# Optimization experiments

Hardware: AMD Instinct MI355X
Metric: run time of the kernel (lower is better)

The kernel has to match this reference:

```python
import jax, jax.numpy as jnp
import numpy as np

P, Q, R, H1, H2, PH, B = 32, 32, 8, 128, 64, 16, 8192
PAIRS = P * Q
OUT = PAIRS * R  # X_Z_layer output units


def _pairwise_mask(p, q, r):
    # rows i*q+k correspond to pair (x_i, z_k): connected to x_i and z_k only
    mx = np.zeros((p * q, p), np.float32)
    for i in range(p):
        mx[i * q:(i + 1) * q, i] = 1.0
    mz = np.tile(np.eye(q, dtype=np.float32), (p, 1))
    m = np.concatenate([mx, mz], axis=1)          # [p*q, p+q]
    return np.repeat(m, r, axis=0)                 # [p*q*r, p+q]


def setup_inputs() -> dict:
    key = jax.random.key(0)
    ks = jax.random.split(key, 24)
    rn = lambda k, s, sc=0.1: jax.random.normal(k, s, jnp.float32) * sc
    x = jax.random.normal(ks[0], (B, P), jnp.float32)
    z = jax.random.normal(ks[1], (B, Q), jnp.float32)
    # X_mlp: P -> H1 -> H2 -> 1
    xw1, xb1 = rn(ks[2], (P, H1)), rn(ks[3], (H1,))
    xw2, xb2 = rn(ks[4], (H1, H2)), rn(ks[5], (H2,))
    xw3, xb3 = rn(ks[6], (H2, 1)), rn(ks[7], (1,))
    # Z_mlp: Q -> H1 -> H2 -> 1
    zw1, zb1 = rn(ks[8], (Q, H1)), rn(ks[9], (H1,))
    zw2, zb2 = rn(ks[10], (Q if False else H1, H2)), rn(ks[11], (H2,))
    zw3, zb3 = rn(ks[12], (H2, 1)), rn(ks[13], (1,))
    # masked X_Z_layer: weight pre-multiplied by structured mask (as in __init__)
    mask = jnp.asarray(_pairwise_mask(P, Q, R))    # [OUT, P+Q]
    xzw = (rn(ks[14], (OUT, P + Q)) * mask).T      # [P+Q, OUT]
    xzb = rn(ks[15], (OUT,))
    # 1024 tiny per-pair MLPs: R -> PH (bias) -> 1 (no bias), stacked
    pw1 = rn(ks[16], (PAIRS, R, PH))
    pb1 = rn(ks[17], (PAIRS, PH))
    pw2 = rn(ks[18], (PAIRS, PH))
    return dict(x=x, z=z, xw1=xw1, xb1=xb1, xw2=xw2, xb2=xb2, xw3=xw3, xb3=xb3,
                zw1=zw1, zb1=zb1, zw2=zw2, zb2=zb2, zw3=zw3, zb3=zb3,
                xzw=xzw, xzb=xzb, pw1=pw1, pb1=pb1, pw2=pw2)


def reference(x, z, xw1, xb1, xw2, xb2, xw3, xb3,
              zw1, zb1, zw2, zb2, zw3, zb3, xzw, xzb, pw1, pb1, pw2):
    relu = jax.nn.relu
    # main-effect MLPs
    hx = relu(relu(x @ xw1 + xb1) @ xw2 + xb2)
    out_x = hx @ xw3 + xb3                         # [B,1]
    hz = relu(relu(z @ zw1 + zb1) @ zw2 + zb2)
    out_z = hz @ zw3 + zb3                         # [B,1]
    # masked interaction layer
    xz = jnp.concatenate([x, z], axis=1)           # [B, P+Q]
    h = relu(xz @ xzw + xzb)                       # [B, OUT]
    # all 1024 per-pair MLPs as one batched GEMM
    hp = h.reshape(h.shape[0], PAIRS, R)           # [B, pairs, R]
    t = relu(jnp.einsum('bpr,prh->bph', hp, pw1) + pb1)
    out_xz = jnp.einsum('bph,ph->b', t, pw2)[:, None]  # sum over pairs -> [B,1]
    return out_x + out_z + out_xz
```

## Files before the change

### kernel.cpp

```cpp
#include <hip/hip_runtime.h>

#define B_TOT 8192
#define PP 32
#define QQ 32
#define RR 8
#define H1 128
#define H2 64
#define PHH 16
#define PAIRS 1024
#define OUT_UNITS 8192

#define NBLK_MM 256
#define NBLK_IA 2048

typedef float f32x16 __attribute__((ext_vector_type(16)));
typedef short s16x8  __attribute__((ext_vector_type(8)));

union FragU { s16x8 v; unsigned int u[4]; };

__device__ inline unsigned int pack_bf16(float lo, float hi) {
    return __builtin_amdgcn_perm(__float_as_uint(hi), __float_as_uint(lo), 0x07060302u);
}

union SharedU {
    union {
        struct {
            float zT[16][256];
            float4 lwx[16][2];
            float4 lwz[16][2];
            float4 lhb[16][2];
            unsigned lpw1T[17][16][4];
            float lpb[16][16];
            float lpw2[16][16];
        } s;
        float red[256][33];
    } ia;
    struct {
        float h1T[128][65];
        float red2[8][64];
    } mm;
};

__global__ __launch_bounds__(512, 4) void fused_k(
    const float* __restrict__ x, const float* __restrict__ z,
    const float* __restrict__ xw1, const float* __restrict__ xb1,
    const float* __restrict__ xw2, const float* __restrict__ xb2,
    const float* __restrict__ xw3, const float* __restrict__ xb3,
    const float* __restrict__ zw1, const float* __restrict__ zb1,
    const float* __restrict__ zw2, const float* __restrict__ zb2,
    const float* __restrict__ zw3, const float* __restrict__ zb3,
    const float* __restrict__ xzw, const float* __restrict__ xzb,
    const float* __restrict__ pw1, const float* __restrict__ pb1,
    const float* __restrict__ pw2, float* __restrict__ out)
{
    __shared__ SharedU sh;
    const int bid  = blockIdx.x;
    const int t    = threadIdx.x;
    const int w    = t >> 6;
    const int lane = t & 63;

    if (bid >= NBLK_MM) {
        const int ib    = bid - NBLK_MM;
        const int bx    = ib & 31;
        const int y     = ib >> 5;
        const int m     = lane & 31;
        const int kh    = lane >> 5;
        const int jj    = m & 15;
        const int cph   = m >> 4;
        const int b0    = bx * 256;
        const int i_x   = y >> 1;
        const int k0    = (y & 1) * 16;
        const int pair0 = y * 16;

        {
            int row = t >> 1;
            int c8  = (t & 1) * 8;
            const float* src = z + (size_t)(b0 + row) * 32 + k0 + c8;
            float4 a4 = *reinterpret_cast<const float4*>(src);
            float4 b4 = *reinterpret_cast<const float4*>(src + 4);
            sh.ia.s.zT[c8+0][row] = a4.x; sh.ia.s.zT[c8+1][row] = a4.y;
            sh.ia.s.zT[c8+2][row] = a4.z; sh.ia.s.zT[c8+3][row] = a4.w;
            sh.ia.s.zT[c8+4][row] = b4.x; sh.ia.s.zT[c8+5][row] = b4.y;
            sh.ia.s.zT[c8+6][row] = b4.z; sh.ia.s.zT[c8+7][row] = b4.w;
        }
        if (t < 128) {
            int p = t >> 3, c = t & 7;
            int gp = pair0 + p;
            reinterpret_cast<float*>(sh.ia.s.lwx)[t] = xzw[(size_t)i_x * OUT_UNITS + gp*8 + c];
            reinterpret_cast<float*>(sh.ia.s.lwz)[t] = xzw[(size_t)(32 + k0 + p) * OUT_UNITS + gp*8 + c];
            reinterpret_cast<float*>(sh.ia.s.lhb)[t] = xzb[gp*8 + c];
        }
        if (t < 256) {
            int p = t >> 4, j = t & 15;
            int gp = pair0 + p;
            sh.ia.s.lpb[p][j]  = pb1[gp*PHH + j];
            sh.ia.s.lpw2[p][j] = pw2[gp*PHH + j];
        }
        #pragma unroll
        for (int it = 0; it < 2; ++it) {
            int idx = t + it * 512;
            int p = idx >> 6, u = (idx >> 4) & 3, j = idx & 15;
            int gp = pair0 + p;
            float lo = pw1[(size_t)gp * 128 + (2*u)*16 + j];
            float hi = pw1[(size_t)gp * 128 + (2*u+1)*16 + j];
            sh.ia.s.lpw1T[p][j][u] = pack_bf16(lo, hi);
        }
        if (t < 64) reinterpret_cast<unsigned*>(sh.ia.s.lpw1T[16])[t] = 0u;

        const int g   = w >> 1;
        const int pph = w & 1;
        const int bl  = g * 64 + m;
        const float xv0 = x[(size_t)(b0 + bl)      * 32 + i_x];
        const float xv1 = x[(size_t)(b0 + bl + 32) * 32 + i_x];
        __syncthreads();

        f32x16 acc0, acc1;
        #pragma unroll
        for (int r = 0; r < 16; ++r) { acc0[r] = 0.f; acc1[r] = 0.f; }

        const bool realB = (kh == cph);

        #pragma unroll 2
        for (int kk = 0; kk < 4; ++kk) {
            const int ppl = pph * 4 + kk;
            const int pAl = 2*ppl + kh;
            const int pBl = 2*ppl + cph;

            const float zv0 = sh.ia.s.zT[pAl][bl];
            const float zv1 = sh.ia.s.zT[pAl][bl + 32];
            const float4 wxa = sh.ia.s.lwx[pAl][0], wxb = sh.ia.s.lwx[pAl][1];
            const float4 wza = sh.ia.s.lwz[pAl][0], wzb = sh.ia.s.lwz[pAl][1];
            const float4 hba = sh.ia.s.lhb[pAl][0], hbb = sh.ia.s.lhb[pAl][1];

            float h0[8], h1v[8];
            h0[0] = fmaxf(fmaf(xv0, wxa.x, fmaf(zv0, wza.x, hba.x)), 0.f);
            h0[1] = fmaxf(fmaf(xv0, wxa.y, fmaf(zv0, wza.y, hba.y)), 0.f);
            h0[2] = fmaxf(fmaf(xv0, wxa.z, fmaf(zv0, wza.z, hba.z)), 0.f);
            h0[3] = fmaxf(fmaf(xv0, wxa.w, fmaf(zv0, wza.w, hba.w)), 0.f);
            h0[4] = fmaxf(fmaf(xv0, wxb.x, fmaf(zv0, wzb.x, hbb.x)), 0.f);
            h0[5] = fmaxf(fmaf(xv0, wxb.y, fmaf(zv0, wzb.y, hbb.y)), 0.f);
            h0[6] = fmaxf(fmaf(xv0, wxb.z, fmaf(zv0, wzb.z, hbb.z)), 0.f);
            h0[7] = fmaxf(fmaf(xv0, wxb.w, fmaf(zv0, wzb.w, hbb.w)), 0.f);
            h1v[0] = fmaxf(fmaf(xv1, wxa.x, fmaf(zv1, wza.x, hba.x)), 0.f);
            h1v[1] = fmaxf(fmaf(xv1, wxa.y, fmaf(zv1, wza.y, hba.y)), 0.f);
            h1v[2] = fmaxf(fmaf(xv1, wxa.z, fmaf(zv1, wza.z, hba.z)), 0.f);
            h1v[3] = fmaxf(fmaf(xv1, wxa.w, fmaf(zv1, wza.w, hba.w)), 0.f);
            h1v[4] = fmaxf(fmaf(xv1, wxb.x, fmaf(zv1, wzb.x, hbb.x)), 0.f);
            h1v[5] = fmaxf(fmaf(xv1, wxb.y, fmaf(zv1, wzb.y, hbb.y)), 0.f);
            h1v[6] = fmaxf(fmaf(xv1, wxb.z, fmaf(zv1, wzb.z, hbb.z)), 0.f);
            h1v[7] = fmaxf(fmaf(xv1, wxb.w, fmaf(zv1, wzb.w, hbb.w)), 0.f);

            FragU a0, a1, bf;
            a0.u[0] = pack_bf16(h0[0], h0[1]);
            a0.u[1] = pack_bf16(h0[2], h0[3]);
            a0.u[2] = pack_bf16(h0[4], h0[5]);
            a0.u[3] = pack_bf16(h0[6], h0[7]);
            a1.u[0] = pack_bf16(h1v[0], h1v[1]);
            a1.u[1] = pack_bf16(h1v[2], h1v[3]);
            a1.u[2] = pack_bf16(h1v[4], h1v[5]);
            a1.u[3] = pack_bf16(h1v[6], h1v[7]);

            const unsigned* bq = sh.ia.s.lpw1T[realB ? pBl : 16][jj];
            bf.u[0] = bq[0]; bf.u[1] = bq[1]; bf.u[2] = bq[2]; bf.u[3] = bq[3];

            const float pbv = sh.ia.s.lpb[pBl][jj];
            const float w2v = sh.ia.s.lpw2[pBl][jj];

            f32x16 cpb;
            #pragma unroll
            for (int r = 0; r < 16; ++r) cpb[r] = pbv;

            f32x16 d0 = __builtin_amdgcn_mfma_f32_32x32x16_bf16(a0.v, bf.v, cpb, 0, 0, 0);
            f32x16 d1 = __builtin_amdgcn_mfma_f32_32x32x16_bf16(a1.v, bf.v, cpb, 0, 0, 0);

            #pragma unroll
            for (int r = 0; r < 16; ++r)
                acc0[r] = fmaf(fmaxf(d0[r], 0.f), w2v, acc0[r]);
            #pragma unroll
            for (int r = 0; r < 16; ++r)
                acc1[r] = fmaf(fmaxf(d1[r], 0.f), w2v, acc1[r]);
        }

        __syncthreads();
        const int rbase = g * 64;
        if (pph == 0) {
            #pragma unroll
            for (int r = 0; r < 16; ++r) {
                int rowf = (r & 3) + 8 * (r >> 2) + 4 * kh;
                sh.ia.red[rbase + rowf][m]      = acc0[r];
                sh.ia.red[rbase + 32 + rowf][m] = acc1[r];
            }
        }
        __syncthreads();
        if (pph == 1) {
            #pragma unroll
            for (int r = 0; r < 16; ++r) {
                int rowf = (r & 3) + 8 * (r >> 2) + 4 * kh;
                sh.ia.red[rbase + rowf][m]      += acc0[r];
                sh.ia.red[rbase + 32 + rowf][m] += acc1[r];
            }
        }
        __syncthreads();
        if (t < 256) {
            float s = 0.f;
            #pragma unroll
            for (int c = 0; c < 32; ++c) s += sh.ia.red[t][c];
            atomicAdd(out + b0 + t, s);
        }
    } else {
        const int btile = bid & 127;
        const int which = bid >> 7;
        const float* in = which ? z   : x;
        const float* w1 = which ? zw1 : xw1;
        const float* b1 = which ? zb1 : xb1;
        const float* w2 = which ? zw2 : xw2;
        const float* b2 = which ? zb2 : xb2;
        const float* w3 = which ? zw3 : xw3;
        const float* b3 = which ? zb3 : xb3;

        const int wu = __builtin_amdgcn_readfirstlane(w);
        const int b0 = btile * 64;

        float xr[32];
        const float4* xrp = reinterpret_cast<const float4*>(in + (size_t)(b0 + lane) * 32);
        #pragma unroll
        for (int q = 0; q < 8; ++q) {
            float4 v = xrp[q];
            xr[4*q] = v.x; xr[4*q+1] = v.y; xr[4*q+2] = v.z; xr[4*q+3] = v.w;
        }

        const int j0 = wu * 16;
        float h1[16];
        #pragma unroll
        for (int j = 0; j < 16; ++j) h1[j] = b1[j0 + j];
        #pragma unroll
        for (int mm = 0; mm < 32; ++mm) {
            float xv = xr[mm];
            #pragma unroll
            for (int j = 0; j < 16; ++j)
                h1[j] = fmaf(xv, w1[mm*H1 + j0 + j], h1[j]);
        }
        #pragma unroll
        for (int j = 0; j < 16; ++j)
            sh.mm.h1T[j0 + j][lane] = fmaxf(h1[j], 0.f);
        __syncthreads();

        const int n0 = __builtin_amdgcn_readfirstlane(wu * 8);
        float h2[8];
        #pragma unroll
        for (int n = 0; n < 8; ++n) h2[n] = b2[n0 + n];
        #pragma unroll 4
        for (int mm = 0; mm < 128; ++mm) {
            float hv = sh.mm.h1T[mm][lane];
            #pragma unroll
            for (int n = 0; n < 8; ++n)
                h2[n] = fmaf(hv, w2[mm*H2 + n0 + n], h2[n]);
        }
        float p = 0.f;
        #pragma unroll
        for (int n = 0; n < 8; ++n)
            p = fmaf(fmaxf(h2[n], 0.f), w3[n0 + n], p);

        sh.mm.red2[wu][lane] = p;
        __syncthreads();
        if (t < 64) {
            float s = b3[0];
            #pragma unroll
            for (int ww = 0; ww < 8; ++ww) s += sh.mm.red2[ww][t];
            atomicAdd(out + b0 + t, s);
        }
    }
}

extern "C" void kernel_launch(void* const* d_in, const int* in_sizes, int n_in,
                              void* d_out, int out_size, void* d_ws, size_t ws_size,
                              hipStream_t stream) {
    const float* x   = (const float*)d_in[0];
    const float* z   = (const float*)d_in[1];
    const float* xw1 = (const float*)d_in[2];
    const float* xb1 = (const float*)d_in[3];
    const float* xw2 = (const float*)d_in[4];
    const float* xb2 = (const float*)d_in[5];
    const float* xw3 = (const float*)d_in[6];
    const float* xb3 = (const float*)d_in[7];
    const float* zw1 = (const float*)d_in[8];
    const float* zb1 = (const float*)d_in[9];
    const float* zw2 = (const float*)d_in[10];
    const float* zb2 = (const float*)d_in[11];
    const float* zw3 = (const float*)d_in[12];
    const float* zb3 = (const float*)d_in[13];
    const float* xzw = (const float*)d_in[14];
    const float* xzb = (const float*)d_in[15];
    const float* pw1 = (const float*)d_in[16];
    const float* pb1 = (const float*)d_in[17];
    const float* pw2 = (const float*)d_in[18];
    float* out = (float*)d_out;

    hipMemsetAsync(out, 0, (size_t)out_size * sizeof(float), stream);

    fused_k<<<dim3(NBLK_MM + NBLK_IA), 512, 0, stream>>>(
        x, z, xw1, xb1, xw2, xb2, xw3, xb3,
        zw1, zb1, zw2, zb2, zw3, zb3,
        xzw, xzb, pw1, pb1, pw2, out);
}
```

Baseline: 130.1 us.

## Remap main-effect MLP threads so lanes own hidden units and waves own batch rows

Restructures the main-effect MLP blocks. Before, each lane owned a batch row and each wave a slice of hidden units, so weights were read as wave-uniform scalars. Now x is staged transposed in shared memory, each lane owns hidden units (two for layer one, one for layer two) and each wave owns 8 batch rows. Weight reads become coalesced per-lane vector loads and activations come in as float4 shared-memory broadcasts. The final reduction runs over 64 hidden units per row from a reused padded buffer, which adds barriers and a longer serial sum in exchange for better weight-load efficiency.

Measured after the change: 125.4 us, median of 2. -3.6%, faster.

```diff
diff --git a/kernel.cpp b/kernel.cpp
--- a/kernel.cpp
+++ b/kernel.cpp
@@ -36,8 +36,10 @@
         float red[256][33];
     } ia;
     struct {
-        float h1T[128][65];
-        float red2[8][64];
+        union {
+            float xT[32][68];
+            float h1T[128][68];
+        };
     } mm;
 };
 
@@ -217,56 +219,86 @@
         const float* b2 = which ? zb2 : xb2;
         const float* w3 = which ? zw3 : xw3;
         const float* b3 = which ? zb3 : xb3;
-
-        const int wu = __builtin_amdgcn_readfirstlane(w);
         const int b0 = btile * 64;
-
-        float xr[32];
-        const float4* xrp = reinterpret_cast<const float4*>(in + (size_t)(b0 + lane) * 32);
+        const int bw = w * 8;
+
+        {
+            int row = t >> 3;
+            int c4  = (t & 7) * 4;
+            float4 v = *reinterpret_cast<const float4*>(in + (size_t)(b0 + row) * 32 + c4);
+            sh.mm.xT[c4+0][row] = v.x; sh.mm.xT[c4+1][row] = v.y;
+            sh.mm.xT[c4+2][row] = v.z; sh.mm.xT[c4+3][row] = v.w;
+        }
+        __syncthreads();
+
+        const int j1 = lane, j2 = lane + 64;
+        float a1[8], a2[8];
+        {
+            float bb1 = b1[j1], bb2 = b1[j2];
+            #pragma unroll
+            for (int i = 0; i < 8; ++i) { a1[i] = bb1; a2[i] = bb2; }
+        }
+        #pragma unroll 4
+        for (int m = 0; m < 32; ++m) {
+            const float4* xr = reinterpret_cast<const float4*>(&sh.mm.xT[m][bw]);
+            float4 xa = xr[0], xb = xr[1];
+            float wv1 = w1[m*H1 + j1];
+            float wv2 = w1[m*H1 + j2];
+            a1[0] = fmaf(xa.x, wv1, a1[0]); a2[0] = fmaf(xa.x, wv2, a2[0]);
+            a1[1] = fmaf(xa.y, wv1, a1[1]); a2[1] = fmaf(xa.y, wv2, a2[1]);
+            a1[2] = fmaf(xa.z, wv1, a1[2]); a2[2] = fmaf(xa.z, wv2, a2[2]);
+            a1[3] = fmaf(xa.w, wv1, a1[3]); a2[3] = fmaf(xa.w, wv2, a2[3]);
+            a1[4] = fmaf(xb.x, wv1, a1[4]); a2[4] = fmaf(xb.x, wv2, a2[4]);
+            a1[5] = fmaf(xb.y, wv1, a1[5]); a2[5] = fmaf(xb.y, wv2, a2[5]);
+            a1[6] = fmaf(xb.z, wv1, a1[6]); a2[6] = fmaf(xb.z, wv2, a2[6]);
+            a1[7] = fmaf(xb.w, wv1, a1[7]); a2[7] = fmaf(xb.w, wv2, a2[7]);
+        }
+        __syncthreads();
         #pragma unroll
-        for (int q = 0; q < 8; ++q) {
-            float4 v = xrp[q];
-            xr[4*q] = v.x; xr[4*q+1] = v.y; xr[4*q+2] = v.z; xr[4*q+3] = v.w;
-        }
-
-        const int j0 = wu * 16;
-        float h1[16];
+        for (int i = 0; i < 8; ++i) {
+            sh.mm.h1T[j1][bw + i] = fmaxf(a1[i], 0.f);
+            sh.mm.h1T[j2][bw + i] = fmaxf(a2[i], 0.f);
+        }
+        __syncthreads();
+
+        float hacc[8];
+        {
+            float b2v = b2[lane];
+            #pragma unroll
+            for (int i = 0; i < 8; ++i) hacc[i] = b2v;
+        }
+        #pragma unroll 4
+        for (int m = 0; m < 128; ++m) {
+            float w2v = w2[m*H2 + lane];
+            const float4* hr = reinterpret_cast<const float4*>(&sh.mm.h1T[m][bw]);
+            float4 ha = hr[0], hb = hr[1];
+            hacc[0] = fmaf(ha.x, w2v, hacc[0]);
+            hacc[1] = fmaf(ha.y, w2v, hacc[1]);
+            hacc[2] = fmaf(ha.z, w2v, hacc[2]);
+            hacc[3] = fmaf(ha.w, w2v, hacc[3]);
+            hacc[4] = fmaf(hb.x, w2v, hacc[4]);
+            hacc[5] = fmaf(hb.y, w2v, hacc[5]);
+            hacc[6] = fmaf(hb.z, w2v, hacc[6]);
+            hacc[7] = fmaf(hb.w, w2v, hacc[7]);
+        }
+        {
+            float w3v = w3[lane];
+            #pragma unroll
+            for (int i = 0; i < 8; ++i) hacc[i] = fmaxf(hacc[i], 0.f) * w3v;
+        }
+        __syncthreads();
         #pragma unroll
-        for (int j = 0; j < 16; ++j) h1[j] = b1[j0 + j];
-        #pragma unroll
-        for (int mm = 0; mm < 32; ++mm) {
-            float xv = xr[mm];
-            #pragma unroll
-            for (int j = 0; j < 16; ++j)
-                h1[j] = fmaf(xv, w1[mm*H1 + j0 + j], h1[j]);
-        }
-        #pragma unroll
-        for (int j = 0; j < 16; ++j)
-            sh.mm.h1T[j0 + j][lane] = fmaxf(h1[j], 0.f);
-        __syncthreads();
-
-        const int n0 = __builtin_amdgcn_readfirstlane(wu * 8);
-        float h2[8];
-        #pragma unroll
-        for (int n = 0; n < 8; ++n) h2[n] = b2[n0 + n];
-        #pragma unroll 4
-        for (int mm = 0; mm < 128; ++mm) {
-            float hv = sh.mm.h1T[mm][lane];
-            #pragma unroll
-            for (int n = 0; n < 8; ++n)
-                h2[n] = fmaf(hv, w2[mm*H2 + n0 + n], h2[n]);
-        }
-        float p = 0.f;
-        #pragma unroll
-        for (int n = 0; n < 8; ++n)
-            p = fmaf(fmaxf(h2[n], 0.f), w3[n0 + n], p);
-
-        sh.mm.red2[wu][lane] = p;
+        for (int i = 0; i < 8; ++i)
+            sh.mm.h1T[bw + i][lane] = hacc[i];
         __syncthreads();
         if (t < 64) {
             float s = b3[0];
-            #pragma unroll
-            for (int ww = 0; ww < 8; ++ww) s += sh.mm.red2[ww][t];
+            const float4* rr = reinterpret_cast<const float4*>(&sh.mm.h1T[t][0]);
+            #pragma unroll
+            for (int c = 0; c < 16; ++c) {
+                float4 v = rr[c];
+                s += (v.x + v.y) + (v.z + v.w);
+            }
             atomicAdd(out + b0 + t, s);
         }
     }
```
